# Performance work log

Hardware: AMD Instinct MI355X
Metric: run time of the kernel (lower is better)

The kernel has to match this reference:

```python
import jax, jax.numpy as jnp
import numpy as np

B, N, D = 64, 128, 512
NEG = 1e30


def _gru_cell(x, h, Wi, Wh, bi, bh):
    # torch nn.GRUCell math
    gi = x @ Wi.T + bi  # (B, 3D)
    gh = h @ Wh.T + bh  # (B, 3D)
    ir, iz, inn = jnp.split(gi, 3, axis=-1)
    hr, hz, hn = jnp.split(gh, 3, axis=-1)
    r = jax.nn.sigmoid(ir + hr)
    z = jax.nn.sigmoid(iz + hz)
    n = jnp.tanh(inn + r * hn)
    return (1.0 - z) * n + z * h


def setup_inputs() -> dict:
    key = jax.random.key(0)
    ks = jax.random.split(key, 16)
    s = 1.0 / np.sqrt(D)
    u = lambda k, shape: jax.random.uniform(k, shape, jnp.float32, -s, s)
    adj = jax.random.randint(ks[13], (B, N, N), 0, 2, jnp.int32)
    adj = adj.at[:, :, 0].set(1)  # ensure each causal prefix has >=1 unmasked edge
    s_mask = jax.random.randint(ks[14], (B, N, N), 0, 2, jnp.int32)
    o_mask = 1 - s_mask
    return {
        "features": jax.random.normal(ks[0], (B, N, D), jnp.float32),
        "Wi_c": u(ks[1], (3 * D, D)),
        "Wh_c": u(ks[2], (3 * D, D)),
        "bi_c": u(ks[3], (3 * D,)),
        "bh_c": u(ks[4], (3 * D,)),
        "Wi_p": u(ks[5], (3 * D, D)),
        "Wh_p": u(ks[6], (3 * D, D)),
        "bi_p": u(ks[7], (3 * D,)),
        "bh_p": u(ks[8], (3 * D,)),
        "lin_w": u(ks[9], (1, 2 * D)),
        "lin_b": u(ks[10], (1,)),
        "Wr0": u(ks[11], (D, D)),
        "Wr1": u(ks[12], (D, D)),
        "adj": adj,
        "s_mask": s_mask,
        "o_mask": o_mask,
    }


def reference(features, Wi_c, Wh_c, bi_c, bh_c, Wi_p, Wh_p, bi_p, bh_p,
              lin_w, lin_b, Wr0, Wr1, adj, s_mask, o_mask):
    dt = features.dtype
    adj_f = adj.astype(dt)
    s_f = s_mask.astype(dt)
    o_f = o_mask.astype(dt)
    wq = lin_w[0, :D]   # applies to Q half of cat(Q, K)
    wk = lin_w[0, D:]   # applies to K half
    b = lin_b[0]
    pos = jnp.arange(N)

    # step 0
    x0 = features[:, 0]
    zeros = jnp.zeros((B, D), dt)
    C0 = _gru_cell(x0, zeros, Wi_c, Wh_c, bi_c, bh_c)
    P0 = _gru_cell(zeros, x0, Wi_p, Wh_p, bi_p, bh_p)
    H0 = jnp.zeros((B, N, D), dt).at[:, 0].set(C0 + P0)

    def step(H, inputs):
        i, x, adj_row, s_row, o_row = inputs
        # masked graph attention over the causal prefix [0, i)
        alpha = (x @ wq)[:, None] + H @ wk + b          # (B, N)
        valid = adj_row * (pos < i).astype(dt)          # (B, N)
        alpha = alpha - (1.0 - valid) * NEG
        w = jax.nn.softmax(alpha, axis=1)               # (B, N)
        V = (H @ Wr0.T) * s_row[:, :, None] + (H @ Wr1.T) * o_row[:, :, None]
        M = jnp.einsum('bn,bnd->bd', w, V)              # (B, D)
        C = _gru_cell(x, M, Wi_c, Wh_c, bi_c, bh_c)
        P = _gru_cell(M, x, Wi_p, Wh_p, bi_p, bh_p)
        H = H.at[:, i].set(C + P)
        return H, None

    xs = (jnp.arange(1, N),
          jnp.swapaxes(features, 0, 1)[1:],
          jnp.swapaxes(adj_f, 0, 1)[1:],
          jnp.swapaxes(s_f, 0, 1)[1:],
          jnp.swapaxes(o_f, 0, 1)[1:])
    H1, _ = jax.lax.scan(step, H0, xs)
    return H1
```

## Files before the change

### kernel.cpp

```cpp
#include <hip/hip_runtime.h>

#define BB 64
#define NN 128
#define DD 512
#define NBLK 128
#define NTHR 512
#define GCOLS 24
#define WCS 2064
#define WXS 1032
#define BCS 6656
#define UBE (BB * 2048)

typedef unsigned short u16;
typedef unsigned int u32;
typedef unsigned long long u64;
typedef __attribute__((ext_vector_type(8))) __bf16 bf16x8;
typedef __attribute__((ext_vector_type(4))) float f32x4;

#define MFMA16(a, b, c) __builtin_amdgcn_mfma_f32_16x16x32_bf16((a), (b), (c), 0, 0, 0)

__device__ __forceinline__ float b2f(u16 u) {
    union { u32 i; float f; } c; c.i = ((u32)u) << 16; return c.f;
}
__device__ __forceinline__ u16 f2b(float f) {
    union { float f; u32 i; } c; c.f = f;
    return (u16)((c.i + 0x7FFFu + ((c.i >> 16) & 1u)) >> 16);
}
__device__ __forceinline__ float sigm(float x) { return 1.f / (1.f + __expf(-x)); }
__device__ __forceinline__ float tanh_(float x) {
    x = fminf(fmaxf(x, -15.f), 15.f);
    float e = __expf(2.f * x);
    return (e - 1.f) / (e + 1.f);
}

__device__ __forceinline__ float ld_cohf(const float* p) {
    return __hip_atomic_load((float*)p, __ATOMIC_RELAXED, __HIP_MEMORY_SCOPE_AGENT);
}
__device__ __forceinline__ void st_cohf(float* p, float v) {
    __hip_atomic_store(p, v, __ATOMIC_RELAXED, __HIP_MEMORY_SCOPE_AGENT);
}
__device__ __forceinline__ void st_cohu32(u32* p, u32 v) {
    __hip_atomic_store(p, v, __ATOMIC_RELAXED, __HIP_MEMORY_SCOPE_AGENT);
}
__device__ __forceinline__ void st_cohi(int* p, int v) {
    __hip_atomic_store(p, v, __ATOMIC_RELAXED, __HIP_MEMORY_SCOPE_AGENT);
}
__device__ __forceinline__ int ld_cohi(int* p) {
    return __hip_atomic_load(p, __ATOMIC_RELAXED, __HIP_MEMORY_SCOPE_AGENT);
}

template<bool CACHED>
__device__ __forceinline__ bf16x8 ldu16(const u16* p) {
    if constexpr (CACHED) {
        return *(const bf16x8*)p;
    } else {
        union { bf16x8 v; u64 q[2]; } u;
        u.q[0] = __hip_atomic_load((u64*)p,     __ATOMIC_RELAXED, __HIP_MEMORY_SCOPE_AGENT);
        u.q[1] = __hip_atomic_load((u64*)p + 1, __ATOMIC_RELAXED, __HIP_MEMORY_SCOPE_AGENT);
        return u.v;
    }
}

__device__ __forceinline__ void gbar(int* sync, int gen, int blk) {
    __syncthreads();
    int* epoch = sync;
    if (blk == 0) {
        const int t = threadIdx.x;
        int done = (t == 0 || t >= NBLK) ? 1 : 0;
        int* myarr = sync + 256 + t * 16;
        int it = 0;
        for (;;) {
            if (!done) {
                int v = ((it & 15) == 15)
                    ? __hip_atomic_load(myarr, __ATOMIC_ACQUIRE, __HIP_MEMORY_SCOPE_AGENT)
                    : __hip_atomic_load(myarr, __ATOMIC_RELAXED, __HIP_MEMORY_SCOPE_AGENT);
                done = (v >= gen);
            }
            ++it;
            if (__syncthreads_and(done)) break;
            __builtin_amdgcn_s_sleep(1);
        }
        if (t == 0) {
            (void)__hip_atomic_load(sync + 256 + 16, __ATOMIC_ACQUIRE, __HIP_MEMORY_SCOPE_AGENT);
            __hip_atomic_store(epoch, gen, __ATOMIC_RELEASE, __HIP_MEMORY_SCOPE_AGENT);
        }
        __syncthreads();
    } else {
        if (threadIdx.x == 0) {
            __hip_atomic_store(sync + 256 + blk * 16, gen, __ATOMIC_RELEASE, __HIP_MEMORY_SCOPE_AGENT);
            int it = 0;
            for (;;) {
                int v = ((it & 15) == 15)
                    ? __hip_atomic_load(epoch, __ATOMIC_ACQUIRE, __HIP_MEMORY_SCOPE_AGENT)
                    : __hip_atomic_load(epoch, __ATOMIC_RELAXED, __HIP_MEMORY_SCOPE_AGENT);
                ++it;
                if (v >= gen) break;
                __builtin_amdgcn_s_sleep(1);
            }
            (void)__hip_atomic_load(epoch, __ATOMIC_ACQUIRE, __HIP_MEMORY_SCOPE_AGENT);
        }
        __syncthreads();
    }
}

__device__ __forceinline__ void gbar_lite(int* flags, int gen, int blk,
                                          int nsig, bool sig, bool wait) {
    __syncthreads();
    if (sig && threadIdx.x == 0)
        st_cohi(flags + blk * 32, gen);
    if (wait) {
        const int t = threadIdx.x;
        int done = (t >= nsig) ? 1 : 0;
        int* f = flags + t * 32;
        for (;;) {
            if (!done) done = (ld_cohi(f) >= gen);
            if (__syncthreads_and(done)) break;
            __builtin_amdgcn_s_sleep(2);
        }
    }
    asm volatile("" ::: "memory");
    __builtin_amdgcn_sched_barrier(0);
}

__device__ __forceinline__ void waitA(int* flagsA, int gen, int grp) {
    const int l = threadIdx.x & 63;
    int* f = flagsA + (grp * 16 + (l & 15)) * 32;
    for (;;) {
        int v = ld_cohi(f);
        if (__all(v >= gen)) break;
        __builtin_amdgcn_s_sleep(1);
    }
    asm volatile("" ::: "memory");
    __builtin_amdgcn_sched_barrier(0);
}

template<bool CACHED>
__device__ __forceinline__ void gates_merged(
    const u16* __restrict__ ub, const u16* s_wc, const float* s_gb,
    float* __restrict__ bc, int blk, int rt, int lr, int lq)
{
    const int cc0 = lr, cc1 = lr + 8;
    const u16* w0 = s_wc + cc0 * WCS;
    const u16* w1 = s_wc + cc1 * WCS;
    const u16* arow = ub + (size_t)(rt * 16 + lr) * 2048;
    f32x4 acc0 = {0.f, 0.f, 0.f, 0.f}, acc1 = {0.f, 0.f, 0.f, 0.f};
    #pragma unroll 4
    for (int c = 0; c < 16; ++c) {
        int kk = c * 32 + lq * 8;
        bf16x8 ah = ldu16<CACHED>(arow + kk);
        bf16x8 al = ldu16<CACHED>(arow + 512 + kk);
        bf16x8 wh0 = *(const bf16x8*)(w0 + kk);
        bf16x8 wl0 = *(const bf16x8*)(w0 + 1024 + kk);
        bf16x8 wh1 = *(const bf16x8*)(w1 + kk);
        bf16x8 wl1 = *(const bf16x8*)(w1 + 1024 + kk);
        acc0 = MFMA16(ah, wh0, acc0); acc0 = MFMA16(al, wh0, acc0); acc0 = MFMA16(ah, wl0, acc0);
        acc1 = MFMA16(ah, wh1, acc1); acc1 = MFMA16(al, wh1, acc1); acc1 = MFMA16(ah, wl1, acc1);
    }
    #pragma unroll 4
    for (int c = 0; c < 16; ++c) {
        int kk = c * 32 + lq * 8;
        bf16x8 ah = ldu16<CACHED>(arow + 1024 + kk);
        bf16x8 al = ldu16<CACHED>(arow + 1536 + kk);
        bf16x8 wh0 = *(const bf16x8*)(w0 + 512 + kk);
        bf16x8 wl0 = *(const bf16x8*)(w0 + 1536 + kk);
        bf16x8 wh1 = *(const bf16x8*)(w1 + 512 + kk);
        bf16x8 wl1 = *(const bf16x8*)(w1 + 1536 + kk);
        acc0 = MFMA16(ah, wh0, acc0); acc0 = MFMA16(al, wh0, acc0); acc0 = MFMA16(ah, wl0, acc0);
        acc1 = MFMA16(ah, wh1, acc1); acc1 = MFMA16(al, wh1, acc1); acc1 = MFMA16(ah, wl1, acc1);
    }
    float b0 = s_gb[cc0], b1 = s_gb[cc1];
    int col0 = blk * GCOLS + cc0, col1 = blk * GCOLS + cc1;
    #pragma unroll
    for (int r = 0; r < 4; ++r) {
        size_t row = (size_t)(rt * 16 + lq * 4 + r) * BCS;
        st_cohf(bc + row + 512 + col0, acc0[r] + b0);
        st_cohf(bc + row + 512 + col1, acc1[r] + b1);
    }
}

__device__ __forceinline__ f32x4 x_core(
    int i, const u16* __restrict__ featblob, const u16* s_wxw,
    int task, int lr, int lq, int* ccO)
{
    const int ct = task & 1, rt = task >> 1;
    const int cc = ct * 8 + lr;
    *ccO = cc;
    const u16* wcol = s_wxw + cc * WXS;
    const u16* arow = featblob + (size_t)(i * 64 + rt * 16 + lr) * 1024;
    f32x4 acc = {0.f, 0.f, 0.f, 0.f};
    #pragma unroll 4
    for (int c = 0; c < 16; ++c) {
        int kk = c * 32 + lq * 8;
        bf16x8 ah = *(const bf16x8*)(arow + kk);
        bf16x8 al = *(const bf16x8*)(arow + 512 + kk);
        bf16x8 wh = *(const bf16x8*)(wcol + kk);
        bf16x8 wl = *(const bf16x8*)(wcol + 512 + kk);
        acc = MFMA16(ah, wh, acc); acc = MFMA16(al, wh, acc); acc = MFMA16(ah, wl, acc);
    }
    return acc;
}

__device__ __forceinline__ void x_task(
    int i, const u16* __restrict__ featblob, const u16* s_wxw, const float* s_xb,
    float* __restrict__ bc, int blk, int task, int lr, int lq)
{
    int cc; f32x4 acc = x_core(i, featblob, s_wxw, task, lr, lq, &cc);
    const int rt = task >> 1;
    const int col = blk * GCOLS + cc;
    float bias = s_xb[cc];
    #pragma unroll
    for (int r = 0; r < 4; ++r)
        st_cohf(bc + (size_t)(rt * 16 + lq * 4 + r) * BCS + 3584 + col, acc[r] + bias);
}

__device__ __forceinline__ void x_task_xg(
    int i, const u16* __restrict__ featblob, const u16* s_wxw, const float* s_xb,
    float* __restrict__ xg, int blk, int task, int lr, int lq)
{
    int cc; f32x4 acc = x_core(i, featblob, s_wxw, task, lr, lq, &cc);
    const int rt = task >> 1;
    const int col = blk * GCOLS + cc;
    float bias = s_xb[cc];
    #pragma unroll
    for (int r = 0; r < 4; ++r)
        xg[((size_t)i * 64 + rt * 16 + lq * 4 + r) * 3072 + col] = acc[r] + bias;
}

template<bool CACHED>
__device__ __forceinline__ void m_task(
    const u16* __restrict__ ub, const u16* __restrict__ WrB,
    float* __restrict__ bc, int blk, int lr, int lq)
{
    const int ct = blk >> 2, rt = blk & 3;
    const int col = ct * 16 + lr;
    const u16* wcol = WrB + (size_t)col * 2048;
    const u16* arow = ub + (size_t)(rt * 16 + lr) * 2048;
    f32x4 acc = {0.f, 0.f, 0.f, 0.f};
    #pragma unroll 4
    for (int c = 0; c < 16; ++c) {
        int kk = c * 32 + lq * 8;
        bf16x8 a0h = ldu16<CACHED>(arow + kk);
        bf16x8 a0l = ldu16<CACHED>(arow + 512 + kk);
        bf16x8 a1h = ldu16<CACHED>(arow + 1024 + kk);
        bf16x8 a1l = ldu16<CACHED>(arow + 1536 + kk);
        bf16x8 w0h = *(const bf16x8*)(wcol + kk);
        bf16x8 w0l = *(const bf16x8*)(wcol + 512 + kk);
        bf16x8 w1h = *(const bf16x8*)(wcol + 1024 + kk);
        bf16x8 w1l = *(const bf16x8*)(wcol + 1536 + kk);
        acc = MFMA16(a0h, w0h, acc); acc = MFMA16(a0l, w0h, acc); acc = MFMA16(a0h, w0l, acc);
        acc = MFMA16(a1h, w1h, acc); acc = MFMA16(a1l, w1h, acc); acc = MFMA16(a1h, w1l, acc);
    }
    #pragma unroll
    for (int r = 0; r < 4; ++r)
        st_cohf(bc + (size_t)(rt * 16 + lq * 4 + r) * BCS + col, acc[r]);
}

__global__ __launch_bounds__(NTHR) void grn_kernel(
    const float* __restrict__ feat, const float* __restrict__ Wi_c, const float* __restrict__ Wh_c,
    const float* __restrict__ bi_c, const float* __restrict__ bh_c,
    const float* __restrict__ Wi_p, const float* __restrict__ Wh_p,
    const float* __restrict__ bi_p, const float* __restrict__ bh_p,
    const float* __restrict__ lin_w, const float* __restrict__ lin_b,
    const float* __restrict__ Wr0, const float* __restrict__ Wr1,
    const int* __restrict__ adj, const int* __restrict__ smask,
    float* __restrict__ out,
    float* __restrict__ q, u16* __restrict__ ublob,
    u16* __restrict__ featblob, float* __restrict__ bc, u16* __restrict__ WrB,
    float* __restrict__ xg, int* __restrict__ sync, int use_ring, int use_xg)
{
    const int t = threadIdx.x, blk = blockIdx.x;
    const int lane = t & 63, wv = t >> 6;
    const int lr = lane & 15, lq = lane >> 4;
    int gen = 0;
    int* flagsA = sync + 4096;
    int* flagsB = sync + 8192;

    __shared__ u16 s_wc[GCOLS * WCS];
    __shared__ __align__(16) char s_wx_raw[GCOLS * WXS * 2];
    __shared__ float s_u0[DD];
    __shared__ float s_ut[DD];
    __shared__ float s_red[NTHR];
    __shared__ float s_hk[NN];
    __shared__ float s_q[NN];
    __shared__ float s_w[NN];
    __shared__ float s_ws[NN];
    __shared__ float s_gb[GCOLS];
    __shared__ float s_xb[GCOLS];

    u16* s_wxw = (u16*)s_wx_raw;
    float* s_wgf = (float*)s_wx_raw;
    float* s_pu = (float*)s_wx_raw;
    float* s_pt = (float*)(s_wx_raw + 6144);
    float* s_scal = (float*)(s_wx_raw + 12288);

    const float wkreg = lin_w[DD + t];

    for (int rr = 0; rr < 64; ++rr) {
        int gr = blk * 64 + rr;
        int bb_ = gr >> 7, nn_ = gr & 127;
        float x = feat[(size_t)gr * DD + t];
        u16 h = f2b(x);
        u16* dst = featblob + (size_t)(nn_ * 64 + bb_) * 1024;
        dst[t] = h;
        dst[512 + t] = f2b(x - b2f(h));
    }
    for (int cc = 0; cc < 4; ++cc) {
        int c = blk * 4 + cc;
        float w0 = Wr0[(size_t)c * DD + t], w1 = Wr1[(size_t)c * DD + t];
        u16 h0 = f2b(w0), h1 = f2b(w1);
        u16* dst = WrB + (size_t)c * 2048;
        dst[t] = h0; dst[512 + t] = f2b(w0 - b2f(h0));
        dst[1024 + t] = h1; dst[1536 + t] = f2b(w1 - b2f(h1));
    }
    {
        float linb = lin_b[0];
        float wqf[8];
        #pragma unroll
        for (int jj = 0; jj < 8; ++jj) wqf[jj] = lin_w[lane * 8 + jj];
        for (int rr = 0; rr < 8; ++rr) {
            int row = blk * 64 + wv * 8 + rr;
            const float* fp = feat + (size_t)row * DD + lane * 8;
            float p = 0.f;
            #pragma unroll
            for (int jj = 0; jj < 8; ++jj) p += fp[jj] * wqf[jj];
            #pragma unroll
            for (int off = 32; off; off >>= 1) p += __shfl_down(p, off, 64);
            if (lane == 0) q[row] = p + linb;
        }
    }
    {
        int jg0 = blk * GCOLS;
        for (int cc = 0; cc < GCOLS; ++cc) {
            int jg = jg0 + cc;
            const float* src = (jg < 1536) ? (Wh_c + (size_t)jg * DD) : (Wi_p + (size_t)(jg - 1536) * DD);
            s_wgf[t * GCOLS + cc] = src[t];
        }
        if (t < GCOLS) {
            int jg = jg0 + t;
            s_gb[t] = (jg < 1536) ? bh_c[jg] : bi_p[jg - 1536];
            s_xb[t] = (jg < 1536) ? bi_c[jg] : bh_p[jg - 1536];
        }
    }
    __syncthreads();
    {
        float acc0[GCOLS], acc1[GCOLS];
        #pragma unroll
        for (int cc = 0; cc < GCOLS; ++cc) { acc0[cc] = 0.f; acc1[cc] = 0.f; }
        for (int j = 0; j < DD; ++j) {
            float wr0 = Wr0[(size_t)j * DD + t];
            float wr1 = Wr1[(size_t)j * DD + t];
            const float* g = s_wgf + j * GCOLS;
            #pragma unroll
            for (int cc = 0; cc < GCOLS; ++cc) {
                float gv = g[cc];
                acc0[cc] += wr0 * gv;
                acc1[cc] += wr1 * gv;
            }
        }
        __syncthreads();
        #pragma unroll
        for (int cc = 0; cc < GCOLS; ++cc) {
            u16 h0 = f2b(acc0[cc]);
            s_wc[cc * WCS + t] = h0;
            s_wc[cc * WCS + 1024 + t] = f2b(acc0[cc] - b2f(h0));
            u16 h1 = f2b(acc1[cc]);
            s_wc[cc * WCS + 512 + t] = h1;
            s_wc[cc * WCS + 1536 + t] = f2b(acc1[cc] - b2f(h1));
        }
    }
    {
        int jx0 = blk * GCOLS;
        for (int cc = 0; cc < GCOLS; ++cc) {
            int jx = jx0 + cc;
            const float* src = (jx < 1536) ? (Wi_c + (size_t)jx * DD) : (Wh_p + (size_t)(jx - 1536) * DD);
            float w = src[t];
            u16 h = f2b(w);
            s_wxw[cc * WXS + t] = h;
            s_wxw[cc * WXS + 512 + t] = f2b(w - b2f(h));
        }
    }
    gbar(sync, ++gen, blk);

    x_task(0, featblob, s_wxw, s_xb, bc, blk, wv, lr, lq);
    if (use_xg) {
        for (int ii = 0; ii < NN; ++ii)
            x_task_xg(ii, featblob, s_wxw, s_xb, xg, blk, wv, lr, lq);
    }
    if (blk < BB && t < NN) s_q[t] = q[blk * NN + t];
    gbar(sync, ++gen, blk);

    if (blk < BB) {
        if (use_xg) {
            s_pu[t] = 0.f; s_pu[512 + t] = 0.f; s_pu[1024 + t] = 0.f;
            s_pt[t] = 0.f; s_pt[512 + t] = 0.f; s_pt[1024 + t] = 0.f;
            if (t == 0) {
                s_scal[0] = -1e30f; s_scal[1] = 0.f;
                s_scal[2] = (float)adj[((size_t)blk * NN + 1) * NN + 0];
                s_scal[3] = (float)smask[((size_t)blk * NN + 1) * NN + 0];
            }
        }
        const float* bcb = bc + (size_t)blk * BCS;
        float ir = ld_cohf(bcb + 3584 + t), iz = ld_cohf(bcb + 4096 + t), inn = ld_cohf(bcb + 4608 + t);
        float r = sigm(ir + bh_c[t]), z = sigm(iz + bh_c[512 + t]);
        float C = (1.f - z) * tanh_(inn + r * bh_c[1024 + t]);
        float ghr = ld_cohf(bcb + 5120 + t), ghz = ld_cohf(bcb + 5632 + t), ghn = ld_cohf(bcb + 6144 + t);
        float r2 = sigm(bi_p[t] + ghr), z2 = sigm(bi_p[512 + t] + ghz);
        float n2 = tanh_(bi_p[1024 + t] + r2 * ghn);
        float x = feat[(size_t)(blk * NN) * DD + t];
        float P = (1.f - z2) * n2 + z2 * x;
        float Hv = C + P;
        out[(size_t)(blk * NN) * DD + t] = Hv;
        s_red[t] = Hv * wkreg;
        __syncthreads();
        if (wv == 0) {
            float p = 0.f;
            #pragma unroll
            for (int jj = 0; jj < 8; ++jj) p += s_red[lane + 64 * jj];
            #pragma unroll
            for (int off = 32; off; off >>= 1) p += __shfl_down(p, off, 64);
            if (lane == 0) s_hk[0] = p;
        }
    }
    gbar(sync, ++gen, blk);

    for (int i = 1; i < NN; ++i) {
        u16* ub_i = ublob + (size_t)(use_ring ? (NN - 1 - i) : 0) * UBE;

        if (blk < BB) {
            if (use_xg) {
                int j = i - 1;
                float Hv;
                if (i >= 2) {
                    const float* bcb = bc + (size_t)blk * BCS;
                    float Mv = ld_cohf(bcb + t);
                    float hr = ld_cohf(bcb + 512 + t), hz = ld_cohf(bcb + 1024 + t), hn = ld_cohf(bcb + 1536 + t);
                    float gir = ld_cohf(bcb + 2048 + t), giz = ld_cohf(bcb + 2560 + t), gin = ld_cohf(bcb + 3072 + t);
                    const float* xrow = xg + ((size_t)j * 64 + blk) * 3072;
                    float ir = xrow[t], iz = xrow[512 + t], inn = xrow[1024 + t];
                    float ghr = xrow[1536 + t], ghz = xrow[2048 + t], ghn = xrow[2560 + t];
                    float x = feat[(size_t)(blk * NN + j) * DD + t];
                    float r = sigm(ir + hr), z = sigm(iz + hz);
                    float C = (1.f - z) * tanh_(inn + r * hn) + z * Mv;
                    float r2 = sigm(gir + ghr), z2 = sigm(giz + ghz);
                    float P = (1.f - z2) * tanh_(gin + r2 * ghn) + z2 * x;
                    Hv = C + P;
                    out[(size_t)(blk * NN + j) * DD + t] = Hv;
                    s_red[t] = Hv * wkreg;
                } else {
                    Hv = out[(size_t)(blk * NN) * DD + t];
                }
                __syncthreads();
                if (wv == 0) {
                    float hk;
                    if (i >= 2) {
                        float p = 0.f;
                        #pragma unroll
                        for (int jj = 0; jj < 8; ++jj) p += s_red[lane + 64 * jj];
                        #pragma unroll
                        for (int off = 32; off; off >>= 1) p += __shfl_down(p, off, 64);
                        if (lane == 0) s_hk[j] = p;
                        hk = p;
                    } else {
                        hk = s_hk[0];
                    }
                    if (lane == 0) {
                        float m_part = s_scal[0], denom_p = s_scal[1];
                        float anew = s_scal[2], snew = s_scal[3];
                        float alpha = s_q[i] + hk;
                        float m = m_part, e_new = 0.f;
                        if (anew != 0.f) { m = fmaxf(m_part, alpha); e_new = __expf(alpha - m); }
                        float scale = __expf(m_part - m);
                        float inv = 1.f / (denom_p * scale + e_new);
                        s_w[0] = scale * inv;
                        s_w[1] = e_new * snew * inv;
                        s_w[2] = e_new * inv;
                    }
                }
                __syncthreads();
                {
                    float u0p = s_pu[t] + s_pu[512 + t] + s_pu[1024 + t];
                    float utp = s_pt[t] + s_pt[512 + t] + s_pt[1024 + t];
                    float CS = s_w[0], C0 = s_w[1], CT = s_w[2];
                    float U0 = u0p * CS + C0 * Hv;
                    float U1 = (utp * CS + CT * Hv) - U0;
                    u16 h0 = f2b(U0); u16 l0 = f2b(U0 - b2f(h0));
                    u16 h1 = f2b(U1); u16 l1 = f2b(U1 - b2f(h1));
                    u32 p0 = (u32)h0 | ((u32)l0 << 16);
                    u32 p1 = (u32)h1 | ((u32)l1 << 16);
                    u32 q0 = (u32)__shfl_xor((int)p0, 1, 64);
                    u32 q1 = (u32)__shfl_xor((int)p1, 1, 64);
                    u32* ub32 = (u32*)(ub_i + (size_t)blk * 2048);
                    int w = t >> 1;
                    if ((t & 1) == 0) {
                        st_cohu32(ub32 + w,       (p0 & 0xFFFFu) | ((q0 & 0xFFFFu) << 16));
                        st_cohu32(ub32 + 256 + w, (p0 >> 16)     | (q0 & 0xFFFF0000u));
                    } else {
                        st_cohu32(ub32 + 512 + w, (q1 & 0xFFFFu) | ((p1 & 0xFFFFu) << 16));
                        st_cohu32(ub32 + 768 + w, (q1 >> 16)     | (p1 & 0xFFFF0000u));
                    }
                }
                __syncthreads();
                if (t == 0) st_cohi(flagsA + blk * 32, i);
            } else {
                int va0 = 0, va1 = 0, vs0 = 0, vs1 = 0;
                float qv = 0.f;
                if (wv == 0) {
                    const int* ar_ = adj + (size_t)(blk * NN + i) * NN;
                    const int* sr_ = smask + (size_t)(blk * NN + i) * NN;
                    va0 = ar_[lane]; va1 = ar_[lane + 64];
                    vs0 = sr_[lane]; vs1 = sr_[lane + 64];
                    qv = s_q[i];
                }
                if (i >= 2) {
                    int j = i - 1;
                    const float* bcb = bc + (size_t)blk * BCS;
                    float Mv = ld_cohf(bcb + t);
                    float hr = ld_cohf(bcb + 512 + t), hz = ld_cohf(bcb + 1024 + t), hn = ld_cohf(bcb + 1536 + t);
                    float gir = ld_cohf(bcb + 2048 + t), giz = ld_cohf(bcb + 2560 + t), gin = ld_cohf(bcb + 3072 + t);
                    float ir = ld_cohf(bcb + 3584 + t), iz = ld_cohf(bcb + 4096 + t), inn = ld_cohf(bcb + 4608 + t);
                    float ghr = ld_cohf(bcb + 5120 + t), ghz = ld_cohf(bcb + 5632 + t), ghn = ld_cohf(bcb + 6144 + t);
                    float x = feat[(size_t)(blk * NN + j) * DD + t];
                    float r = sigm(ir + hr), z = sigm(iz + hz);
                    float C = (1.f - z) * tanh_(inn + r * hn) + z * Mv;
                    float r2 = sigm(gir + ghr), z2 = sigm(giz + ghz);
                    float P = (1.f - z2) * tanh_(gin + r2 * ghn) + z2 * x;
                    float Hv = C + P;
                    out[(size_t)(blk * NN + j) * DD + t] = Hv;
                    s_red[t] = Hv * wkreg;
                }
                s_u0[t] = 0.f; s_ut[t] = 0.f;
                __syncthreads();
                if (wv == 0) {
                    if (i >= 2) {
                        float p = 0.f;
                        #pragma unroll
                        for (int jj = 0; jj < 8; ++jj) p += s_red[lane + 64 * jj];
                        #pragma unroll
                        for (int off = 32; off; off >>= 1) p += __shfl_down(p, off, 64);
                        if (lane == 0) s_hk[i - 1] = p;
                    }
                    int n2i = lane + 64;
                    float a0 = (lane < i && va0 != 0) ? (qv + s_hk[lane]) : -1e30f;
                    float a1 = (n2i < i && va1 != 0) ? (qv + s_hk[n2i]) : -1e30f;
                    float m = fmaxf(a0, a1);
                    #pragma unroll
                    for (int off = 32; off; off >>= 1) m = fmaxf(m, __shfl_xor(m, off, 64));
                    float e0 = (a0 > -1e29f) ? __expf(a0 - m) : 0.f;
                    float e1 = (a1 > -1e29f) ? __expf(a1 - m) : 0.f;
                    float ss = e0 + e1;
                    #pragma unroll
                    for (int off = 32; off; off >>= 1) ss += __shfl_xor(ss, off, 64);
                    float inv = 1.f / ss;
                    float w0 = e0 * inv, w1 = e1 * inv;
                    s_w[lane] = w0; s_w[n2i] = w1;
                    s_ws[lane] = w0 * (float)vs0;
                    s_ws[n2i] = w1 * (float)vs1;
                }
                __syncthreads();
                {
                    int g = t >> 7, dqb = (t & 127) * 4;
                    const float* Hb = out + (size_t)blk * NN * DD + dqb;
                    f32x4 u0 = {0.f, 0.f, 0.f, 0.f}, ut = {0.f, 0.f, 0.f, 0.f};
                    int n = g;
                    for (; n + 12 < i; n += 16) {
                        f32x4 h0 = *(const f32x4*)(Hb + (size_t)n * DD);
                        f32x4 h1 = *(const f32x4*)(Hb + (size_t)(n + 4) * DD);
                        f32x4 h2 = *(const f32x4*)(Hb + (size_t)(n + 8) * DD);
                        f32x4 h3 = *(const f32x4*)(Hb + (size_t)(n + 12) * DD);
                        u0 += s_ws[n] * h0 + s_ws[n + 4] * h1 + s_ws[n + 8] * h2 + s_ws[n + 12] * h3;
                        ut += s_w[n] * h0 + s_w[n + 4] * h1 + s_w[n + 8] * h2 + s_w[n + 12] * h3;
                    }
                    for (; n < i; n += 4) {
                        f32x4 h0 = *(const f32x4*)(Hb + (size_t)n * DD);
                        u0 += s_ws[n] * h0;
                        ut += s_w[n] * h0;
                    }
                    #pragma unroll
                    for (int e = 0; e < 4; ++e) {
                        atomicAdd(&s_u0[dqb + e], u0[e]);
                        atomicAdd(&s_ut[dqb + e], ut[e]);
                    }
                }
                __syncthreads();
                {
                    int tt = t & 255, sel = t >> 8;
                    float a0 = s_u0[2 * tt], a1 = s_u0[2 * tt + 1];
                    float t0_ = s_ut[2 * tt], t1_ = s_ut[2 * tt + 1];
                    float b0_ = t0_ - a0, b1_ = t1_ - a1;
                    float v0 = sel ? b0_ : a0, v1 = sel ? b1_ : a1;
                    u16 h0 = f2b(v0), h1 = f2b(v1);
                    u16 l0 = f2b(v0 - b2f(h0)), l1 = f2b(v1 - b2f(h1));
                    u32 hw = (u32)h0 | ((u32)h1 << 16);
                    u32 lw = (u32)l0 | ((u32)l1 << 16);
                    u32* ub32 = (u32*)(ub_i + (size_t)blk * 2048);
                    int base = sel * 512;
                    st_cohu32(ub32 + base + tt, hw);
                    st_cohu32(ub32 + base + 256 + tt, lw);
                }
                __syncthreads();
                if (t == 0) st_cohi(flagsA + blk * 32, i);
            }
        }

        if (use_xg) {
            if (wv < 4) {
                waitA(flagsA, i, wv);
                if (use_ring) gates_merged<true >(ub_i, s_wc, s_gb, bc, blk, wv, lr, lq);
                else          gates_merged<false>(ub_i, s_wc, s_gb, bc, blk, wv, lr, lq);
            } else if (wv == 7) {
                waitA(flagsA, i, blk & 3);
                if (use_ring) m_task<true >(ub_i, WrB, bc, blk, lr, lq);
                else          m_task<false>(ub_i, WrB, bc, blk, lr, lq);
            } else if (blk < BB && i + 1 < NN) {
                const int ii = i + 1;
                const int w = wv - 4;
                const int* ar = adj + (size_t)(blk * NN + ii) * NN;
                const int* sr = smask + (size_t)(blk * NN + ii) * NN;
                int a0 = ar[lane], a1 = ar[lane + 64];
                int s0 = sr[lane], s1 = sr[lane + 64];
                float qv = s_q[ii];
                float al0 = (lane < i && a0 != 0) ? (qv + s_hk[lane]) : -1e30f;
                float al1 = (lane + 64 < i && a1 != 0) ? (qv + s_hk[lane + 64]) : -1e30f;
                float m = fmaxf(al0, al1);
                #pragma unroll
                for (int off = 32; off; off >>= 1) m = fmaxf(m, __shfl_xor(m, off, 64));
                float e0 = (al0 > -1e29f) ? __expf(al0 - m) : 0.f;
                float e1 = (al1 > -1e29f) ? __expf(al1 - m) : 0.f;
                float es0 = e0 * (float)s0, es1 = e1 * (float)s1;
                const float* Hb = out + (size_t)blk * NN * DD + lane * 8;
                f32x4 pa = {0.f,0.f,0.f,0.f}, pb = {0.f,0.f,0.f,0.f};
                f32x4 ta = {0.f,0.f,0.f,0.f}, tb = {0.f,0.f,0.f,0.f};
                for (int n = w; n < i; n += 3) {
                    float en  = __shfl((n < 64) ? e0 : e1, n & 63, 64);
                    float esn = __shfl((n < 64) ? es0 : es1, n & 63, 64);
                    f32x4 h0 = *(const f32x4*)(Hb + (size_t)n * DD);
                    f32x4 h1 = *(const f32x4*)(Hb + (size_t)n * DD + 4);
                    pa += esn * h0; pb += esn * h1;
                    ta += en * h0;  tb += en * h1;
                }
                *(f32x4*)&s_pu[w * 512 + lane * 8]     = pa;
                *(f32x4*)&s_pu[w * 512 + lane * 8 + 4] = pb;
                *(f32x4*)&s_pt[w * 512 + lane * 8]     = ta;
                *(f32x4*)&s_pt[w * 512 + lane * 8 + 4] = tb;
                if (w == 0) {
                    float ds = e0 + e1;
                    #pragma unroll
                    for (int off = 32; off; off >>= 1) ds += __shfl_xor(ds, off, 64);
                    if (lane == 0) {
                        s_scal[0] = m; s_scal[1] = ds;
                        s_scal[2] = (float)ar[i];
                        s_scal[3] = (float)sr[i];
                    }
                }
                if (w == 2) {
                    const float* fp = feat + (size_t)(blk * NN + i) * DD + lane * 8;
                    f32x4 f0 = *(const f32x4*)fp;
                    f32x4 f1 = *(const f32x4*)(fp + 4);
                    const float* xp = xg + ((size_t)i * 64 + blk) * 3072 + lane * 16;
                    float x0 = xp[0], x1 = xp[1024], x2 = xp[2048];
                    asm volatile("" :: "v"(f0), "v"(f1), "v"(x0), "v"(x1), "v"(x2));
                }
            }
        } else {
            if (wv < 4) {
                waitA(flagsA, i, wv);
                gates_merged<false>(ub_i, s_wc, s_gb, bc, blk, wv, lr, lq);
            } else if (wv == 4) {
                x_task(i, featblob, s_wxw, s_xb, bc, blk, 0, lr, lq);
                x_task(i, featblob, s_wxw, s_xb, bc, blk, 1, lr, lq);
                x_task(i, featblob, s_wxw, s_xb, bc, blk, 2, lr, lq);
            } else if (wv == 5) {
                x_task(i, featblob, s_wxw, s_xb, bc, blk, 3, lr, lq);
                x_task(i, featblob, s_wxw, s_xb, bc, blk, 4, lr, lq);
                x_task(i, featblob, s_wxw, s_xb, bc, blk, 5, lr, lq);
            } else if (wv == 6) {
                x_task(i, featblob, s_wxw, s_xb, bc, blk, 6, lr, lq);
                x_task(i, featblob, s_wxw, s_xb, bc, blk, 7, lr, lq);
            } else {
                waitA(flagsA, i, blk & 3);
                m_task<false>(ub_i, WrB, bc, blk, lr, lq);
            }
        }

        gbar_lite(flagsB, i, blk, NBLK, true, blk < BB);
    }

    if (blk < BB) {
        int j = NN - 1;
        const float* bcb = bc + (size_t)blk * BCS;
        float Mv = ld_cohf(bcb + t);
        float hr = ld_cohf(bcb + 512 + t), hz = ld_cohf(bcb + 1024 + t), hn = ld_cohf(bcb + 1536 + t);
        float gir = ld_cohf(bcb + 2048 + t), giz = ld_cohf(bcb + 2560 + t), gin = ld_cohf(bcb + 3072 + t);
        float ir, iz, inn, ghr, ghz, ghn;
        if (use_xg) {
            const float* xrow = xg + ((size_t)j * 64 + blk) * 3072;
            ir = xrow[t]; iz = xrow[512 + t]; inn = xrow[1024 + t];
            ghr = xrow[1536 + t]; ghz = xrow[2048 + t]; ghn = xrow[2560 + t];
        } else {
            ir = ld_cohf(bcb + 3584 + t); iz = ld_cohf(bcb + 4096 + t); inn = ld_cohf(bcb + 4608 + t);
            ghr = ld_cohf(bcb + 5120 + t); ghz = ld_cohf(bcb + 5632 + t); ghn = ld_cohf(bcb + 6144 + t);
        }
        float x = feat[(size_t)(blk * NN + j) * DD + t];
        float r = sigm(ir + hr), z = sigm(iz + hz);
        float C = (1.f - z) * tanh_(inn + r * hn) + z * Mv;
        float r2 = sigm(gir + ghr), z2 = sigm(giz + ghz);
        float P = (1.f - z2) * tanh_(gin + r2 * ghn) + z2 * x;
        out[(size_t)(blk * NN + j) * DD + t] = C + P;
    }
}

extern "C" void kernel_launch(void* const* d_in, const int* in_sizes, int n_in,
                              void* d_out, int out_size, void* d_ws, size_t ws_size,
                              hipStream_t stream) {
    (void)in_sizes; (void)n_in; (void)out_size;
    const float* feat = (const float*)d_in[0];
    const float* Wi_c = (const float*)d_in[1];
    const float* Wh_c = (const float*)d_in[2];
    const float* bi_c = (const float*)d_in[3];
    const float* bh_c = (const float*)d_in[4];
    const float* Wi_p = (const float*)d_in[5];
    const float* Wh_p = (const float*)d_in[6];
    const float* bi_p = (const float*)d_in[7];
    const float* bh_p = (const float*)d_in[8];
    const float* lin_w = (const float*)d_in[9];
    const float* lin_b = (const float*)d_in[10];
    const float* Wr0 = (const float*)d_in[11];
    const float* Wr1 = (const float*)d_in[12];
    const int* adj = (const int*)d_in[13];
    const int* smask = (const int*)d_in[14];
    float* out = (float*)d_out;

    char* ws = (char*)d_ws;
    size_t off = 0;
    int* sync_ = (int*)(ws + off);      off += 65536;
    float* q = (float*)(ws + off);      off += (size_t)BB * NN * 4;
    u16* featblob = (u16*)(ws + off);   off += (size_t)BB * NN * 1024 * 2;
    float* bc = (float*)(ws + off);     off += (size_t)BB * BCS * 4;
    u16* WrB = (u16*)(ws + off);        off += (size_t)512 * 2048 * 2;
    u16* ublob = (u16*)(ws + off);
    size_t ring_bytes = (size_t)(NN - 1) * UBE * 2;
    size_t xg_bytes = (size_t)NN * 64 * 3072 * 4;
    int use_ring = (ws_size >= off + ring_bytes) ? 1 : 0;
    float* xg = (float*)(ws + off + ring_bytes);
    int use_xg = (use_ring && ws_size >= off + ring_bytes + xg_bytes) ? 1 : 0;

    (void)hipMemsetAsync(d_ws, 0, 65536, stream);
    hipLaunchKernelGGL(grn_kernel, dim3(NBLK), dim3(NTHR), 0, stream,
                       feat, Wi_c, Wh_c, bi_c, bh_c, Wi_p, Wh_p, bi_p, bh_p,
                       lin_w, lin_b, Wr0, Wr1, adj, smask, out,
                       q, ublob, featblob, bc, WrB, xg, sync_, use_ring, use_xg);
}
```

Baseline: 3.418 ms.

## Replace per-block flag polling with atomic counters and transpose MFMA tiles for packed stores

```diff
diff --git a/kernel.cpp b/kernel.cpp
--- a/kernel.cpp
+++ b/kernel.cpp
@@ -42,11 +42,25 @@
 __device__ __forceinline__ void st_cohu32(u32* p, u32 v) {
     __hip_atomic_store(p, v, __ATOMIC_RELAXED, __HIP_MEMORY_SCOPE_AGENT);
 }
+__device__ __forceinline__ void st_cohu64(u64* p, u64 v) {
+    __hip_atomic_store(p, v, __ATOMIC_RELAXED, __HIP_MEMORY_SCOPE_AGENT);
+}
 __device__ __forceinline__ void st_cohi(int* p, int v) {
     __hip_atomic_store(p, v, __ATOMIC_RELAXED, __HIP_MEMORY_SCOPE_AGENT);
 }
 __device__ __forceinline__ int ld_cohi(int* p) {
     return __hip_atomic_load(p, __ATOMIC_RELAXED, __HIP_MEMORY_SCOPE_AGENT);
+}
+__device__ __forceinline__ void ctr_add(int* p) {
+    (void)__hip_atomic_fetch_add(p, 1, __ATOMIC_RELAXED, __HIP_MEMORY_SCOPE_AGENT);
+}
+__device__ __forceinline__ void ctr_wait(int* p, int tgt) {
+    for (;;) {
+        if (ld_cohi(p) >= tgt) break;
+        __builtin_amdgcn_s_sleep(1);
+    }
+    asm volatile("" ::: "memory");
+    __builtin_amdgcn_sched_barrier(0);
 }
 
 template<bool CACHED>
@@ -121,7 +135,6 @@
     asm volatile("" ::: "memory");
     __builtin_amdgcn_sched_barrier(0);
 }
-
 __device__ __forceinline__ void waitA(int* flagsA, int gen, int grp) {
     const int l = threadIdx.x & 63;
     int* f = flagsA + (grp * 16 + (l & 15)) * 32;
@@ -132,6 +145,123 @@
     }
     asm volatile("" ::: "memory");
     __builtin_amdgcn_sched_barrier(0);
+}
+
+__device__ __forceinline__ void gates_t(
+    const u16* __restrict__ ub, const u16* s_wc, const float* s_gb,
+    float* __restrict__ bc, int blk, int rt, int lr, int lq)
+{
+    const int cA0 = lr;
+    const int cA1 = 16 + (lr & 7);
+    const u16* w0 = s_wc + cA0 * WCS;
+    const u16* w1 = s_wc + cA1 * WCS;
+    const u16* arow = ub + (size_t)(rt * 16 + lr) * 2048;
+    f32x4 acc0 = {0.f,0.f,0.f,0.f}, acc1 = {0.f,0.f,0.f,0.f};
+    #pragma unroll 4
+    for (int c = 0; c < 16; ++c) {
+        int kk = c * 32 + lq * 8;
+        bf16x8 ah = *(const bf16x8*)(arow + kk);
+        bf16x8 al = *(const bf16x8*)(arow + 512 + kk);
+        bf16x8 wh0 = *(const bf16x8*)(w0 + kk);
+        bf16x8 wl0 = *(const bf16x8*)(w0 + 1024 + kk);
+        bf16x8 wh1 = *(const bf16x8*)(w1 + kk);
+        bf16x8 wl1 = *(const bf16x8*)(w1 + 1024 + kk);
+        acc0 = MFMA16(wh0, ah, acc0); acc0 = MFMA16(wh0, al, acc0); acc0 = MFMA16(wl0, ah, acc0);
+        acc1 = MFMA16(wh1, ah, acc1); acc1 = MFMA16(wh1, al, acc1); acc1 = MFMA16(wl1, ah, acc1);
+    }
+    #pragma unroll 4
+    for (int c = 0; c < 16; ++c) {
+        int kk = c * 32 + lq * 8;
+        bf16x8 ah = *(const bf16x8*)(arow + 1024 + kk);
+        bf16x8 al = *(const bf16x8*)(arow + 1536 + kk);
+        bf16x8 wh0 = *(const bf16x8*)(w0 + 512 + kk);
+        bf16x8 wl0 = *(const bf16x8*)(w0 + 1536 + kk);
+        bf16x8 wh1 = *(const bf16x8*)(w1 + 512 + kk);
+        bf16x8 wl1 = *(const bf16x8*)(w1 + 1536 + kk);
+        acc0 = MFMA16(wh0, ah, acc0); acc0 = MFMA16(wh0, al, acc0); acc0 = MFMA16(wl0, ah, acc0);
+        acc1 = MFMA16(wh1, ah, acc1); acc1 = MFMA16(wh1, al, acc1); acc1 = MFMA16(wl1, ah, acc1);
+    }
+    const int row = rt * 16 + lr;
+    float* dst = bc + (size_t)row * BCS + 512 + blk * GCOLS;
+    const int c0 = lq * 4;
+    union { float f[2]; u64 u; } pk;
+    pk.f[0] = acc0[0] + s_gb[c0];     pk.f[1] = acc0[1] + s_gb[c0 + 1];
+    st_cohu64((u64*)(dst + c0), pk.u);
+    pk.f[0] = acc0[2] + s_gb[c0 + 2]; pk.f[1] = acc0[3] + s_gb[c0 + 3];
+    st_cohu64((u64*)(dst + c0 + 2), pk.u);
+    if (lq < 2) {
+        const int c1 = 16 + lq * 4;
+        pk.f[0] = acc1[0] + s_gb[c1];     pk.f[1] = acc1[1] + s_gb[c1 + 1];
+        st_cohu64((u64*)(dst + c1), pk.u);
+        pk.f[0] = acc1[2] + s_gb[c1 + 2]; pk.f[1] = acc1[3] + s_gb[c1 + 3];
+        st_cohu64((u64*)(dst + c1 + 2), pk.u);
+    }
+}
+
+__device__ __forceinline__ void m_task_t(
+    const u16* __restrict__ ub, const u16* __restrict__ WrB,
+    float* __restrict__ bc, int blk, int lr, int lq)
+{
+    const int ct = blk >> 2, rt = blk & 3;
+    const u16* wcol = WrB + (size_t)(ct * 16 + lr) * 2048;
+    const u16* arow = ub + (size_t)(rt * 16 + lr) * 2048;
+    f32x4 acc = {0.f,0.f,0.f,0.f};
+    #pragma unroll 4
+    for (int c = 0; c < 16; ++c) {
+        int kk = c * 32 + lq * 8;
+        bf16x8 a0h = *(const bf16x8*)(arow + kk);
+        bf16x8 a0l = *(const bf16x8*)(arow + 512 + kk);
+        bf16x8 a1h = *(const bf16x8*)(arow + 1024 + kk);
+        bf16x8 a1l = *(const bf16x8*)(arow + 1536 + kk);
+        bf16x8 w0h = *(const bf16x8*)(wcol + kk);
+        bf16x8 w0l = *(const bf16x8*)(wcol + 512 + kk);
+        bf16x8 w1h = *(const bf16x8*)(wcol + 1024 + kk);
+        bf16x8 w1l = *(const bf16x8*)(wcol + 1536 + kk);
+        acc = MFMA16(w0h, a0h, acc); acc = MFMA16(w0h, a0l, acc); acc = MFMA16(w0l, a0h, acc);
+        acc = MFMA16(w1h, a1h, acc); acc = MFMA16(w1h, a1l, acc); acc = MFMA16(w1l, a1h, acc);
+    }
+    const int row = rt * 16 + lr;
+    float* dst = bc + (size_t)row * BCS + ct * 16 + lq * 4;
+    union { float f[2]; u64 u; } pk;
+    pk.f[0] = acc[0]; pk.f[1] = acc[1];
+    st_cohu64((u64*)dst, pk.u);
+    pk.f[0] = acc[2]; pk.f[1] = acc[3];
+    st_cohu64((u64*)(dst + 2), pk.u);
+}
+
+__device__ __forceinline__ void x_xg_t(
+    int i, const u16* __restrict__ featblob, const u16* s_wxw, const float* s_xb,
+    float* __restrict__ xg, int blk, int rt, int lr, int lq)
+{
+    const int cA0 = lr, cA1 = 16 + (lr & 7);
+    const u16* w0 = s_wxw + cA0 * WXS;
+    const u16* w1 = s_wxw + cA1 * WXS;
+    const u16* arow = featblob + (size_t)(i * 64 + rt * 16 + lr) * 1024;
+    f32x4 acc0 = {0.f,0.f,0.f,0.f}, acc1 = {0.f,0.f,0.f,0.f};
+    #pragma unroll 4
+    for (int c = 0; c < 16; ++c) {
+        int kk = c * 32 + lq * 8;
+        bf16x8 ah = *(const bf16x8*)(arow + kk);
+        bf16x8 al = *(const bf16x8*)(arow + 512 + kk);
+        bf16x8 wh0 = *(const bf16x8*)(w0 + kk);
+        bf16x8 wl0 = *(const bf16x8*)(w0 + 512 + kk);
+        bf16x8 wh1 = *(const bf16x8*)(w1 + kk);
+        bf16x8 wl1 = *(const bf16x8*)(w1 + 512 + kk);
+        acc0 = MFMA16(wh0, ah, acc0); acc0 = MFMA16(wh0, al, acc0); acc0 = MFMA16(wl0, ah, acc0);
+        acc1 = MFMA16(wh1, ah, acc1); acc1 = MFMA16(wh1, al, acc1); acc1 = MFMA16(wl1, ah, acc1);
+    }
+    const int row = rt * 16 + lr;
+    float* dst = xg + ((size_t)i * 64 + row) * 3072 + blk * GCOLS;
+    const int c0 = lq * 4;
+    f32x4 v0 = { acc0[0] + s_xb[c0], acc0[1] + s_xb[c0 + 1],
+                 acc0[2] + s_xb[c0 + 2], acc0[3] + s_xb[c0 + 3] };
+    *(f32x4*)(dst + c0) = v0;
+    if (lq < 2) {
+        const int c1 = 16 + lq * 4;
+        f32x4 v1 = { acc1[0] + s_xb[c1], acc1[1] + s_xb[c1 + 1],
+                     acc1[2] + s_xb[c1 + 2], acc1[3] + s_xb[c1 + 3] };
+        *(f32x4*)(dst + c1) = v1;
+    }
 }
 
 template<bool CACHED>
@@ -143,7 +273,7 @@
     const u16* w0 = s_wc + cc0 * WCS;
     const u16* w1 = s_wc + cc1 * WCS;
     const u16* arow = ub + (size_t)(rt * 16 + lr) * 2048;
-    f32x4 acc0 = {0.f, 0.f, 0.f, 0.f}, acc1 = {0.f, 0.f, 0.f, 0.f};
+    f32x4 acc0 = {0.f,0.f,0.f,0.f}, acc1 = {0.f,0.f,0.f,0.f};
     #pragma unroll 4
     for (int c = 0; c < 16; ++c) {
         int kk = c * 32 + lq * 8;
@@ -187,7 +317,7 @@
     *ccO = cc;
     const u16* wcol = s_wxw + cc * WXS;
     const u16* arow = featblob + (size_t)(i * 64 + rt * 16 + lr) * 1024;
-    f32x4 acc = {0.f, 0.f, 0.f, 0.f};
+    f32x4 acc = {0.f,0.f,0.f,0.f};
     #pragma unroll 4
     for (int c = 0; c < 16; ++c) {
         int kk = c * 32 + lq * 8;
@@ -213,19 +343,6 @@
         st_cohf(bc + (size_t)(rt * 16 + lq * 4 + r) * BCS + 3584 + col, acc[r] + bias);
 }
 
-__device__ __forceinline__ void x_task_xg(
-    int i, const u16* __restrict__ featblob, const u16* s_wxw, const float* s_xb,
-    float* __restrict__ xg, int blk, int task, int lr, int lq)
-{
-    int cc; f32x4 acc = x_core(i, featblob, s_wxw, task, lr, lq, &cc);
-    const int rt = task >> 1;
-    const int col = blk * GCOLS + cc;
-    float bias = s_xb[cc];
-    #pragma unroll
-    for (int r = 0; r < 4; ++r)
-        xg[((size_t)i * 64 + rt * 16 + lq * 4 + r) * 3072 + col] = acc[r] + bias;
-}
-
 template<bool CACHED>
 __device__ __forceinline__ void m_task(
     const u16* __restrict__ ub, const u16* __restrict__ WrB,
@@ -235,7 +352,7 @@
     const int col = ct * 16 + lr;
     const u16* wcol = WrB + (size_t)col * 2048;
     const u16* arow = ub + (size_t)(rt * 16 + lr) * 2048;
-    f32x4 acc = {0.f, 0.f, 0.f, 0.f};
+    f32x4 acc = {0.f,0.f,0.f,0.f};
     #pragma unroll 4
     for (int c = 0; c < 16; ++c) {
         int kk = c * 32 + lq * 8;
@@ -383,8 +500,9 @@
 
     x_task(0, featblob, s_wxw, s_xb, bc, blk, wv, lr, lq);
     if (use_xg) {
-        for (int ii = 0; ii < NN; ++ii)
-            x_task_xg(ii, featblob, s_wxw, s_xb, xg, blk, wv, lr, lq);
+        int i0 = (wv >> 2) * 64;
+        for (int ii = i0; ii < i0 + 64; ++ii)
+            x_xg_t(ii, featblob, s_wxw, s_xb, xg, blk, wv & 3, lr, lq);
     }
     if (blk < BB && t < NN) s_q[t] = q[blk * NN + t];
     gbar(sync, ++gen, blk);
@@ -426,8 +544,11 @@
     for (int i = 1; i < NN; ++i) {
         u16* ub_i = ublob + (size_t)(use_ring ? (NN - 1 - i) : 0) * UBE;
 
-        if (blk < BB) {
-            if (use_xg) {
+        if (use_xg) {
+            int* scA = sync + 4096 + (i - 1) * 64;
+            int* cB  = sync + 12288 + (i - 1) * 16;
+
+            if (blk < BB) {
                 int j = i - 1;
                 float Hv;
                 if (i >= 2) {
@@ -500,8 +621,81 @@
                     }
                 }
                 __syncthreads();
-                if (t == 0) st_cohi(flagsA + blk * 32, i);
+                if (t == 0) ctr_add(scA + (blk >> 4) * 16);
+
+                if (wv < 4) {
+                    ctr_wait(scA + wv * 16, 16);
+                    gates_t(ub_i, s_wc, s_gb, bc, blk, wv, lr, lq);
+                } else if (wv == 7) {
+                    ctr_wait(scA + (blk & 3) * 16, 16);
+                    m_task_t(ub_i, WrB, bc, blk, lr, lq);
+                } else if (i + 1 < NN) {
+                    const int ii = i + 1;
+                    const int w = wv - 4;
+                    const int* ar = adj + (size_t)(blk * NN + ii) * NN;
+                    const int* sr = smask + (size_t)(blk * NN + ii) * NN;
+                    int a0 = ar[lane], a1 = ar[lane + 64];
+                    int s0 = sr[lane], s1 = sr[lane + 64];
+                    float qv = s_q[ii];
+                    float al0 = (lane < i && a0 != 0) ? (qv + s_hk[lane]) : -1e30f;
+                    float al1 = (lane + 64 < i && a1 != 0) ? (qv + s_hk[lane + 64]) : -1e30f;
+                    float m = fmaxf(al0, al1);
+                    #pragma unroll
+                    for (int off = 32; off; off >>= 1) m = fmaxf(m, __shfl_xor(m, off, 64));
+                    float e0 = (al0 > -1e29f) ? __expf(al0 - m) : 0.f;
+                    float e1 = (al1 > -1e29f) ? __expf(al1 - m) : 0.f;
+                    float es0 = e0 * (float)s0, es1 = e1 * (float)s1;
+                    const float* Hb = out + (size_t)blk * NN * DD + lane * 8;
+                    f32x4 pa = {0.f,0.f,0.f,0.f}, pb = {0.f,0.f,0.f,0.f};
+                    f32x4 ta = {0.f,0.f,0.f,0.f}, tb = {0.f,0.f,0.f,0.f};
+                    for (int n = w; n < i; n += 3) {
+                        float en  = __shfl((n < 64) ? e0 : e1, n & 63, 64);
+                        float esn = __shfl((n < 64) ? es0 : es1, n & 63, 64);
+                        f32x4 h0 = *(const f32x4*)(Hb + (size_t)n * DD);
+                        f32x4 h1 = *(const f32x4*)(Hb + (size_t)n * DD + 4);
+                        pa += esn * h0; pb += esn * h1;
+                        ta += en * h0;  tb += en * h1;
+                    }
+                    *(f32x4*)&s_pu[w * 512 + lane * 8]     = pa;
+                    *(f32x4*)&s_pu[w * 512 + lane * 8 + 4] = pb;
+                    *(f32x4*)&s_pt[w * 512 + lane * 8]     = ta;
+                    *(f32x4*)&s_pt[w * 512 + lane * 8 + 4] = tb;
+                    if (w == 0) {
+                        float ds = e0 + e1;
+                        #pragma unroll
+                        for (int off = 32; off; off >>= 1) ds += __shfl_xor(ds, off, 64);
+                        if (lane == 0) {
+                            s_scal[0] = m; s_scal[1] = ds;
+                            s_scal[2] = (float)ar[i];
+                            s_scal[3] = (float)sr[i];
+                        }
+                    }
+                    if (w == 2) {
+                        const float* fp = feat + (size_t)(blk * NN + i) * DD + lane * 8;
+                        f32x4 f0 = *(const f32x4*)fp;
+                        f32x4 f1 = *(const f32x4*)(fp + 4);
+                        const float* xp = xg + ((size_t)i * 64 + blk) * 3072 + lane * 16;
+                        float x0 = xp[0], x1 = xp[1024], x2 = xp[2048];
+                        asm volatile("" :: "v"(f0), "v"(f1), "v"(x0), "v"(x1), "v"(x2));
+                    }
+                }
+                __syncthreads();
+                if (t == 0) ctr_add(cB);
+                if (wv == 0) ctr_wait(cB, NBLK);
+                __syncthreads();
             } else {
+                if (wv < 4) {
+                    ctr_wait(scA + wv * 16, 16);
+                    gates_t(ub_i, s_wc, s_gb, bc, blk, wv, lr, lq);
+                } else if (wv == 7) {
+                    ctr_wait(scA + (blk & 3) * 16, 16);
+                    m_task_t(ub_i, WrB, bc, blk, lr, lq);
+                }
+                __syncthreads();
+                if (t == 0) ctr_add(cB);
+            }
+        } else {
+            if (blk < BB) {
                 int va0 = 0, va1 = 0, vs0 = 0, vs1 = 0;
                 float qv = 0.f;
                 if (wv == 0) {
@@ -560,7 +754,7 @@
                 {
                     int g = t >> 7, dqb = (t & 127) * 4;
                     const float* Hb = out + (size_t)blk * NN * DD + dqb;
-                    f32x4 u0 = {0.f, 0.f, 0.f, 0.f}, ut = {0.f, 0.f, 0.f, 0.f};
+                    f32x4 u0 = {0.f,0.f,0.f,0.f}, ut = {0.f,0.f,0.f,0.f};
                     int n = g;
                     for (; n + 12 < i; n += 16) {
                         f32x4 h0 = *(const f32x4*)(Hb + (size_t)n * DD);
@@ -600,68 +794,6 @@
                 __syncthreads();
                 if (t == 0) st_cohi(flagsA + blk * 32, i);
             }
-        }
-
-        if (use_xg) {
-            if (wv < 4) {
-                waitA(flagsA, i, wv);
-                if (use_ring) gates_merged<true >(ub_i, s_wc, s_gb, bc, blk, wv, lr, lq);
-                else          gates_merged<false>(ub_i, s_wc, s_gb, bc, blk, wv, lr, lq);
-            } else if (wv == 7) {
-                waitA(flagsA, i, blk & 3);
-                if (use_ring) m_task<true >(ub_i, WrB, bc, blk, lr, lq);
-                else          m_task<false>(ub_i, WrB, bc, blk, lr, lq);
-            } else if (blk < BB && i + 1 < NN) {
-                const int ii = i + 1;
-                const int w = wv - 4;
-                const int* ar = adj + (size_t)(blk * NN + ii) * NN;
-                const int* sr = smask + (size_t)(blk * NN + ii) * NN;
-                int a0 = ar[lane], a1 = ar[lane + 64];
-                int s0 = sr[lane], s1 = sr[lane + 64];
-                float qv = s_q[ii];
-                float al0 = (lane < i && a0 != 0) ? (qv + s_hk[lane]) : -1e30f;
-                float al1 = (lane + 64 < i && a1 != 0) ? (qv + s_hk[lane + 64]) : -1e30f;
-                float m = fmaxf(al0, al1);
-                #pragma unroll
-                for (int off = 32; off; off >>= 1) m = fmaxf(m, __shfl_xor(m, off, 64));
-                float e0 = (al0 > -1e29f) ? __expf(al0 - m) : 0.f;
-                float e1 = (al1 > -1e29f) ? __expf(al1 - m) : 0.f;
-                float es0 = e0 * (float)s0, es1 = e1 * (float)s1;
-                const float* Hb = out + (size_t)blk * NN * DD + lane * 8;
-                f32x4 pa = {0.f,0.f,0.f,0.f}, pb = {0.f,0.f,0.f,0.f};
-                f32x4 ta = {0.f,0.f,0.f,0.f}, tb = {0.f,0.f,0.f,0.f};
-                for (int n = w; n < i; n += 3) {
-                    float en  = __shfl((n < 64) ? e0 : e1, n & 63, 64);
-                    float esn = __shfl((n < 64) ? es0 : es1, n & 63, 64);
-                    f32x4 h0 = *(const f32x4*)(Hb + (size_t)n * DD);
-                    f32x4 h1 = *(const f32x4*)(Hb + (size_t)n * DD + 4);
-                    pa += esn * h0; pb += esn * h1;
-                    ta += en * h0;  tb += en * h1;
-                }
-                *(f32x4*)&s_pu[w * 512 + lane * 8]     = pa;
-                *(f32x4*)&s_pu[w * 512 + lane * 8 + 4] = pb;
-                *(f32x4*)&s_pt[w * 512 + lane * 8]     = ta;
-                *(f32x4*)&s_pt[w * 512 + lane * 8 + 4] = tb;
-                if (w == 0) {
-                    float ds = e0 + e1;
-                    #pragma unroll
-                    for (int off = 32; off; off >>= 1) ds += __shfl_xor(ds, off, 64);
-                    if (lane == 0) {
-                        s_scal[0] = m; s_scal[1] = ds;
-                        s_scal[2] = (float)ar[i];
-                        s_scal[3] = (float)sr[i];
-                    }
-                }
-                if (w == 2) {
-                    const float* fp = feat + (size_t)(blk * NN + i) * DD + lane * 8;
-                    f32x4 f0 = *(const f32x4*)fp;
-                    f32x4 f1 = *(const f32x4*)(fp + 4);
-                    const float* xp = xg + ((size_t)i * 64 + blk) * 3072 + lane * 16;
-                    float x0 = xp[0], x1 = xp[1024], x2 = xp[2048];
-                    asm volatile("" :: "v"(f0), "v"(f1), "v"(x0), "v"(x1), "v"(x2));
-                }
-            }
-        } else {
             if (wv < 4) {
                 waitA(flagsA, i, wv);
                 gates_merged<false>(ub_i, s_wc, s_gb, bc, blk, wv, lr, lq);
@@ -680,9 +812,8 @@
                 waitA(flagsA, i, blk & 3);
                 m_task<false>(ub_i, WrB, bc, blk, lr, lq);
             }
-        }
-
-        gbar_lite(flagsB, i, blk, NBLK, true, blk < BB);
+            gbar_lite(flagsB, i, blk, NBLK, true, blk < BB);
+        }
     }
 
     if (blk < BB) {
```

Result: slower. 3.557 ms (+4.1%).
